# Optimization experiments

Measured on AMD Instinct MI355X. Metric: run time of the kernel, lower is better.

## Reference

```python
import jax, jax.numpy as jnp
import numpy as np

D_MODEL = 256
N_LAYERS = 2
EXPAND = 2
D_INNER = EXPAND * D_MODEL  # 512
D_STATE = 16
D_CONV = 4
DT_RANK = max(1, D_MODEL // 16)  # 16


def _selective_scan(x, dt, B, C, A, D):
    # x, dt: [b, l, d]   B, C: [b, l, n]   A: [d, n]   D: [d]
    dA = jnp.exp(jnp.einsum('bld,dn->bldn', dt, A))          # discretized state matrix
    dBx = jnp.einsum('bld,bln,bld->bldn', dt, B, x)           # dt * B * u

    def step(h, inp):
        dA_t, dBx_t, C_t = inp                                 # [b,d,n],[b,d,n],[b,n]
        h = dA_t * h + dBx_t
        y = jnp.einsum('bdn,bn->bd', h, C_t)
        return h, y

    h0 = jnp.zeros((x.shape[0], A.shape[0], A.shape[1]), x.dtype)
    _, ys = jax.lax.scan(step, h0, (jnp.moveaxis(dA, 1, 0),
                                    jnp.moveaxis(dBx, 1, 0),
                                    jnp.moveaxis(C, 1, 0)))
    return jnp.moveaxis(ys, 0, 1) + x * D                      # [b, l, d]


def _mamba_block(z, in_w, conv_w, conv_b, xp_w, dt_w, dt_b, A_log, Dp, out_w):
    b, l, _ = z.shape
    xz = z @ in_w.T                                            # [b, l, 2*d_inner]
    x, gate = jnp.split(xz, 2, axis=-1)
    # causal depthwise conv1d over time
    xt = jnp.transpose(x, (0, 2, 1))                            # [b, d_inner, l]
    xt = jax.lax.conv_general_dilated(
        xt, conv_w[:, None, :], window_strides=(1,),
        padding=[(D_CONV - 1, 0)], feature_group_count=D_INNER)
    x = jax.nn.silu(jnp.transpose(xt, (0, 2, 1)) + conv_b)      # [b, l, d_inner]
    x_dbl = x @ xp_w.T                                          # [b, l, dt_rank + 2*d_state]
    dt, Bm, Cm = jnp.split(x_dbl, [DT_RANK, DT_RANK + D_STATE], axis=-1)
    dt = jax.nn.softplus(dt @ dt_w.T + dt_b)                    # [b, l, d_inner]
    A = -jnp.exp(A_log)                                         # [d_inner, d_state]
    y = _selective_scan(x, dt, Bm, Cm, A, Dp)
    y = y * jax.nn.silu(gate)
    return y @ out_w.T                                          # [b, l, d_model]


def setup_inputs() -> dict:
    key = jax.random.key(0)
    ks = jax.random.split(key, 9)
    B, L = 2, 4096
    z = jax.random.normal(ks[0], (B, L, D_MODEL), jnp.float32)
    s = 0.02
    in_proj_w = jax.random.normal(ks[1], (N_LAYERS, 2 * D_INNER, D_MODEL), jnp.float32) * s
    conv_w = jax.random.normal(ks[2], (N_LAYERS, D_INNER, D_CONV), jnp.float32) * 0.2
    conv_b = jnp.zeros((N_LAYERS, D_INNER), jnp.float32)
    x_proj_w = jax.random.normal(ks[3], (N_LAYERS, DT_RANK + 2 * D_STATE, D_INNER), jnp.float32) * s
    dt_proj_w = jax.random.normal(ks[4], (N_LAYERS, D_INNER, DT_RANK), jnp.float32) * 0.1
    dt_proj_b = jax.random.uniform(ks[5], (N_LAYERS, D_INNER), jnp.float32, -4.0, -2.0)
    A_log = jnp.log(jnp.broadcast_to(jnp.arange(1, D_STATE + 1, dtype=jnp.float32),
                                     (N_LAYERS, D_INNER, D_STATE)))
    D_param = jnp.ones((N_LAYERS, D_INNER), jnp.float32)
    out_proj_w = jax.random.normal(ks[6], (N_LAYERS, D_MODEL, D_INNER), jnp.float32) * s
    return {"z": z, "in_proj_w": in_proj_w, "conv_w": conv_w, "conv_b": conv_b,
            "x_proj_w": x_proj_w, "dt_proj_w": dt_proj_w, "dt_proj_b": dt_proj_b,
            "A_log": A_log, "D_param": D_param, "out_proj_w": out_proj_w}


def reference(z, in_proj_w, conv_w, conv_b, x_proj_w, dt_proj_w, dt_proj_b,
              A_log, D_param, out_proj_w):
    for i in range(N_LAYERS):
        z = _mamba_block(z, in_proj_w[i], conv_w[i], conv_b[i], x_proj_w[i],
                         dt_proj_w[i], dt_proj_b[i], A_log[i], D_param[i], out_proj_w[i])
    return z
```

## Files before the change

### kernel.cpp

```cpp
#include <hip/hip_runtime.h>
#include <hip/hip_bf16.h>
#include <cstdint>
#include <cstddef>

#define DM   256
#define DI   512
#define DS   16
#define LSEQ 4096
#define BATCH 2
#define BLROWS (BATCH * LSEQ)
#define NCH  128
#define CLEN 32
#define XCP  520

#define OFF_INW 0
#define OFF_XC  0
#define OFF_Z   65536
#define OFF_XD  65536
#define OFF_XX  90880
#define SMEM_SZ 127280

typedef __bf16 bf16x8 __attribute__((ext_vector_type(8)));
typedef float  f32x4  __attribute__((ext_vector_type(4)));
typedef unsigned short u16;
typedef u16 u16x8 __attribute__((ext_vector_type(8)));
typedef u16 u16x4 __attribute__((ext_vector_type(4)));

__device__ __forceinline__ u16 f2bfu(float f) {
    union { float f; unsigned u; } c; c.f = f;
    unsigned u = c.u;
    return (u16)((u + 0x7fffu + ((u >> 16) & 1u)) >> 16);
}
__device__ __forceinline__ float bfu2f(u16 u) {
    union { unsigned u; float f; } c; c.u = ((unsigned)u) << 16; return c.f;
}
__device__ __forceinline__ float siluf(float v) {
    return v * (1.0f / (1.0f + __expf(-v)));
}
__device__ __forceinline__ void gload_lds16(const void* g, void* l) {
    __builtin_amdgcn_global_load_lds(
        (const __attribute__((address_space(1))) unsigned int*)g,
        (__attribute__((address_space(3))) unsigned int*)l, 16, 0, 0);
}

#define N_INW  (2*1024*256)
#define N_OUTW (2*256*512)
#define N_XPW  (2*64*512)
#define N_Z    (BLROWS*DM)
__global__ __launch_bounds__(256) void cast_all_k(
    const float* __restrict__ in_w, const float* __restrict__ out_w,
    const float* __restrict__ xp_w, const float* __restrict__ z,
    u16* __restrict__ inw_bf, u16* __restrict__ outw_bf,
    u16* __restrict__ xpw_bf, u16* __restrict__ z_bf) {
    int i = blockIdx.x * 256 + threadIdx.x;
    if (i < N_INW) {
        inw_bf[i] = f2bfu(in_w[i]);
    } else if (i < N_INW + N_OUTW) {
        int j = i - N_INW;
        outw_bf[j] = f2bfu(out_w[j]);
    } else if (i < N_INW + N_OUTW + N_XPW) {
        int j = i - (N_INW + N_OUTW);
        int k = j & 511, o = (j >> 9) & 63, l = j >> 15;
        xpw_bf[j] = f2bfu((o < 48) ? xp_w[(l * 48 + o) * 512 + k] : 0.0f);
    } else {
        int j = i - (N_INW + N_OUTW + N_XPW);
        z_bf[j] = f2bfu(z[j]);
    }
}

__global__ __launch_bounds__(512) void fused_a_k(
    const u16* __restrict__ zin, const u16* __restrict__ inw,
    const float* __restrict__ cw, const float* __restrict__ cb,
    const __bf16* __restrict__ xpw,
    const float* __restrict__ dtw, const float* __restrict__ dtb,
    const float* __restrict__ Alog,
    u16* __restrict__ xcb, u16* __restrict__ dtob, u16* __restrict__ gateb,
    float* __restrict__ BCg, u16* __restrict__ Pb, u16* __restrict__ Sb) {
    __shared__ __align__(16) char smem[SMEM_SZ];
    u16*  inw_s = (u16*)(smem + OFF_INW);
    u16*  z_s   = (u16*)(smem + OFF_Z);
    u16*  xx_s  = (u16*)(smem + OFF_XX);
    u16*  xc_s  = (u16*)(smem + OFF_XC);
    float* xd_s = (float*)(smem + OFF_XD);
    int tid = threadIdx.x;
    int c = blockIdx.x, b = blockIdx.y;
    int bl0 = b * LSEQ + c * CLEN;
    int wave = tid >> 6, lane = tid & 63;
    int row = lane & 15, q = lane >> 4;
    int d = tid;

    for (int idx = tid; idx < 48 * 32; idx += 512) {
        int r = idx >> 5, c8 = idx & 31;
        u16x8 v = {0,0,0,0,0,0,0,0};
        if (r < 35 && (c > 0 || r >= 3))
            v = *(const u16x8*)(zin + (size_t)(bl0 - 3 + r) * DM + c8 * 8);
        *(u16x8*)(z_s + r * 264 + c8 * 8) = v;
    }
    __syncthreads();

    for (int g = 0; g < 8; ++g) {
        {
            int pos = lane & 31, roff = lane >> 5;
            #pragma unroll
            for (int i = 0; i < 8; ++i) {
                int r_abs = wave * 16 + i * 2 + roff;
                int chunk = (pos - r_abs) & 31;
                gload_lds16(inw + (size_t)(g * 128 + r_abs) * 256 + chunk * 8,
                            inw_s + (wave * 16 + i * 2) * 256);
            }
        }
        __syncthreads();
        f32x4 acc[3] = {};
        #pragma unroll
        for (int kb = 0; kb < 8; ++kb) {
            int cidx = kb * 4 + q;
            int r_abs = wave * 16 + row;
            int pos = (cidx + r_abs) & 31;
            bf16x8 bb = *(const bf16x8*)(inw_s + r_abs * 256 + pos * 8);
            #pragma unroll
            for (int mt = 0; mt < 3; ++mt) {
                bf16x8 a = *(const bf16x8*)(z_s + (mt*16 + row) * 264 + kb*32 + q*8);
                acc[mt] = __builtin_amdgcn_mfma_f32_16x16x32_bf16(a, bb, acc[mt], 0, 0, 0);
            }
        }
        __syncthreads();
        int col = g * 128 + wave * 16 + row;
        #pragma unroll
        for (int mt = 0; mt < 3; ++mt)
            #pragma unroll
            for (int r = 0; r < 4; ++r) {
                int grow = mt * 16 + q * 4 + r;
                if (g < 4) {
                    if (grow < 35) xx_s[grow * XCP + col] = f2bfu(acc[mt][r]);
                } else {
                    int t = grow - 3;
                    if (t >= 0 && t < CLEN)
                        gateb[(size_t)(bl0 + t) * DI + (col - 512)] = f2bfu(acc[mt][r]);
                }
            }
    }
    __syncthreads();

    {
        float w0 = cw[d*4], w1 = cw[d*4+1], w2 = cw[d*4+2], w3 = cw[d*4+3];
        float bias = cb[d];
        float xm3 = bfu2f(xx_s[0*XCP + d]);
        float xm2 = bfu2f(xx_s[1*XCP + d]);
        float xm1 = bfu2f(xx_s[2*XCP + d]);
        #pragma unroll 4
        for (int t = 0; t < CLEN; ++t) {
            float xcur = bfu2f(xx_s[(t + 3) * XCP + d]);
            float v = siluf(fmaf(w0, xm3, fmaf(w1, xm2, fmaf(w2, xm1, fmaf(w3, xcur, bias)))));
            u16 vb = f2bfu(v);
            xc_s[t * XCP + d] = vb;
            xcb[(size_t)(bl0 + t) * DI + d] = vb;
            xm3 = xm2; xm2 = xm1; xm1 = xcur;
        }
    }
    __syncthreads();

    {
        int mt = wave & 1, nt = wave >> 1;
        f32x4 acc = {0.f, 0.f, 0.f, 0.f};
        #pragma unroll
        for (int kb = 0; kb < 16; ++kb) {
            bf16x8 a = *(const bf16x8*)&xc_s[(mt*16 + row) * XCP + kb*32 + q*8];
            bf16x8 bb = *(const bf16x8*)(xpw + (size_t)(nt*16 + row) * 512 + kb*32 + q*8);
            acc = __builtin_amdgcn_mfma_f32_16x16x32_bf16(a, bb, acc, 0, 0, 0);
        }
        #pragma unroll
        for (int r = 0; r < 4; ++r)
            xd_s[(mt*16 + q*4 + r) * 68 + nt*16 + row] = acc[r];
    }
    __syncthreads();

    for (int i = tid; i < CLEN * 32; i += 512) {
        int t = i >> 5, cc = i & 31;
        BCg[((size_t)(b*NCH + c) * CLEN + t) * 32 + cc] = xd_s[t*68 + 16 + cc];
    }

    {
        float dtwr[16];
        const f32x4* w4 = (const f32x4*)(dtw + (size_t)d * 16);
        #pragma unroll
        for (int g = 0; g < 4; ++g) { f32x4 v = w4[g];
            dtwr[g*4] = v[0]; dtwr[g*4+1] = v[1]; dtwr[g*4+2] = v[2]; dtwr[g*4+3] = v[3]; }
        float dtbv = dtb[d];
        float Ac[16];
        const f32x4* a4 = (const f32x4*)(Alog + (size_t)d * 16);
        #pragma unroll
        for (int g = 0; g < 4; ++g) { f32x4 v = a4[g];
            #pragma unroll
            for (int j = 0; j < 4; ++j) Ac[g*4+j] = -__expf(v[j]); }
        bool fastp = true;
        #pragma unroll
        for (int n = 1; n < 16; ++n)
            fastp = fastp && (fabsf(Ac[n] - (float)(n+1) * Ac[0]) <= 1e-4f * fabsf(Ac[n]));
        float p[16], s[16];
        #pragma unroll
        for (int n = 0; n < 16; ++n) { p[n] = 1.0f; s[n] = 0.0f; }
        for (int t = 0; t < CLEN; ++t) {
            float acc = dtbv;
            #pragma unroll
            for (int r = 0; r < 16; ++r) acc = fmaf(xd_s[t*68 + r], dtwr[r], acc);
            float dtv = (acc > 20.0f) ? acc : logf(1.0f + __expf(acc));
            dtob[(size_t)(bl0 + t) * DI + d] = f2bfu(dtv);
            float xv = bfu2f(xc_s[t * XCP + d]);
            float dx = dtv * xv;
            float an[16];
            if (fastp) {
                float a0 = __expf(dtv * Ac[0]);
                an[0] = a0;
                #pragma unroll
                for (int n = 1; n < 16; ++n) an[n] = an[n-1] * a0;
            } else {
                #pragma unroll
                for (int n = 0; n < 16; ++n) an[n] = __expf(dtv * Ac[n]);
            }
            #pragma unroll
            for (int n = 0; n < 16; ++n) {
                s[n] = fmaf(an[n], s[n], xd_s[t*68 + 16 + n] * dx);
                p[n] *= an[n];
            }
        }
        size_t base = ((size_t)(b*NCH + c) * DI + d) * 16;
        u16x8 pv0, pv1, sv0, sv1;
        #pragma unroll
        for (int n = 0; n < 8; ++n) {
            pv0[n] = f2bfu(p[n]);   pv1[n] = f2bfu(p[8+n]);
            sv0[n] = f2bfu(s[n]);   sv1[n] = f2bfu(s[8+n]);
        }
        *(u16x8*)(Pb + base)     = pv0;  *(u16x8*)(Pb + base + 8) = pv1;
        *(u16x8*)(Sb + base)     = sv0;  *(u16x8*)(Sb + base + 8) = sv1;
    }
}

__global__ __launch_bounds__(256) void scanB_k(
    const u16* __restrict__ Pb, const u16* __restrict__ Sb,
    float* __restrict__ H) {
    int i = blockIdx.x * 256 + threadIdx.x;
    int b = i >> 11, j4 = i & 2047;
    f32x4 h = {0.f, 0.f, 0.f, 0.f};
    for (int c = 0; c < NCH; ++c) {
        size_t i4 = (size_t)(b*NCH + c) * 2048 + j4;
        u16x4 pv = ((const u16x4*)Pb)[i4];
        u16x4 sv = ((const u16x4*)Sb)[i4];
        ((f32x4*)H)[i4] = h;
        #pragma unroll
        for (int j = 0; j < 4; ++j) h[j] = fmaf(bfu2f(pv[j]), h[j], bfu2f(sv[j]));
    }
}

__global__ __launch_bounds__(512) void fused_c_k(
    const u16* __restrict__ xcb, const u16* __restrict__ dtob,
    const float* __restrict__ BCg, const float* __restrict__ H,
    const float* __restrict__ Alog, const float* __restrict__ Dp,
    const u16* __restrict__ gateb, const __bf16* __restrict__ outw,
    u16* __restrict__ Ob, float* __restrict__ Of) {
    __shared__ u16 y_s[CLEN * XCP];
    __shared__ float BCs[CLEN * 32];
    int tid = threadIdx.x;
    int c = blockIdx.x, b = blockIdx.y;
    int bl0 = b * LSEQ + c * CLEN;
    int d = tid;

    for (int i = tid; i < CLEN * 32; i += 512)
        BCs[i] = BCg[(size_t)(b*NCH + c) * (CLEN*32) + i];

    float Ac[16], h[16];
    {
        const f32x4* a4 = (const f32x4*)(Alog + (size_t)d * 16);
        const f32x4* h4 = (const f32x4*)(H + ((size_t)(b*NCH + c) * DI + d) * 16);
        #pragma unroll
        for (int g = 0; g < 4; ++g) {
            f32x4 av = a4[g]; f32x4 hv = h4[g];
            #pragma unroll
            for (int j = 0; j < 4; ++j) { Ac[g*4+j] = -__expf(av[j]); h[g*4+j] = hv[j]; }
        }
    }
    bool fastp = true;
    #pragma unroll
    for (int n = 1; n < 16; ++n)
        fastp = fastp && (fabsf(Ac[n] - (float)(n+1) * Ac[0]) <= 1e-4f * fabsf(Ac[n]));
    float Dv = Dp[d];
    __syncthreads();

    #pragma unroll 4
    for (int t = 0; t < CLEN; ++t) {
        float dtv = bfu2f(dtob[(size_t)(bl0 + t) * DI + d]);
        float xv  = bfu2f(xcb[(size_t)(bl0 + t) * DI + d]);
        float gv  = bfu2f(gateb[(size_t)(bl0 + t) * DI + d]);
        float dx = dtv * xv;
        float an[16];
        if (fastp) {
            float a0 = __expf(dtv * Ac[0]);
            an[0] = a0;
            #pragma unroll
            for (int n = 1; n < 16; ++n) an[n] = an[n-1] * a0;
        } else {
            #pragma unroll
            for (int n = 0; n < 16; ++n) an[n] = __expf(dtv * Ac[n]);
        }
        float y = 0.f;
        #pragma unroll
        for (int n = 0; n < 16; ++n) {
            h[n] = fmaf(an[n], h[n], BCs[t*32 + n] * dx);
            y = fmaf(h[n], BCs[t*32 + 16 + n], y);
        }
        float yv = fmaf(xv, Dv, y) * siluf(gv);
        y_s[t * XCP + d] = f2bfu(yv);
    }
    __syncthreads();

    {
        int wave = tid >> 6, lane = tid & 63;
        int row = lane & 15, q = lane >> 4;
        int mt = wave & 1, ng = wave >> 1;
        f32x4 acc[4] = {};
        #pragma unroll
        for (int kb = 0; kb < 16; ++kb) {
            bf16x8 a = *(const bf16x8*)&y_s[(mt*16 + row) * XCP + kb*32 + q*8];
            #pragma unroll
            for (int ni = 0; ni < 4; ++ni) {
                bf16x8 bb = *(const bf16x8*)(outw +
                    (size_t)(ng*64 + ni*16 + row) * 512 + kb*32 + q*8);
                acc[ni] = __builtin_amdgcn_mfma_f32_16x16x32_bf16(a, bb, acc[ni], 0, 0, 0);
            }
        }
        #pragma unroll
        for (int r = 0; r < 4; ++r) {
            size_t gr = (size_t)(bl0 + mt*16 + q*4 + r) * DM;
            #pragma unroll
            for (int ni = 0; ni < 4; ++ni) {
                int gc = ng*64 + ni*16 + row;
                if (Ob) Ob[gr + gc] = f2bfu(acc[ni][r]);
                else    Of[gr + gc] = acc[ni][r];
            }
        }
    }
}

extern "C" void kernel_launch(void* const* d_in, const int* in_sizes, int n_in,
                              void* d_out, int out_size, void* d_ws, size_t ws_size,
                              hipStream_t stream) {
    (void)in_sizes; (void)n_in; (void)out_size; (void)ws_size;
    const float* z_in   = (const float*)d_in[0];
    const float* in_w   = (const float*)d_in[1];
    const float* conv_w = (const float*)d_in[2];
    const float* conv_b = (const float*)d_in[3];
    const float* xp_w   = (const float*)d_in[4];
    const float* dt_w   = (const float*)d_in[5];
    const float* dt_b   = (const float*)d_in[6];
    const float* A_log  = (const float*)d_in[7];
    const float* D_par  = (const float*)d_in[8];
    const float* out_w  = (const float*)d_in[9];
    float* outp = (float*)d_out;

    char* p = (char*)d_ws;
    auto alloc = [&](size_t bytes) { char* r = p; p += (bytes + 255) & ~(size_t)255; return r; };
    u16* z_bf    = (u16*)alloc((size_t)BLROWS*DM*2);
    u16* z2_bf   = (u16*)alloc((size_t)BLROWS*DM*2);
    u16* xc_bf   = (u16*)alloc((size_t)BLROWS*DI*2);
    u16* dt_bf   = (u16*)alloc((size_t)BLROWS*DI*2);
    u16* gate_bf = (u16*)alloc((size_t)BLROWS*DI*2);
    u16* inw_bf  = (u16*)alloc((size_t)2*1024*256*2);
    u16* outw_bf = (u16*)alloc((size_t)2*256*512*2);
    u16* xpw_bf  = (u16*)alloc((size_t)2*64*512*2);
    float* BCg   = (float*)alloc((size_t)BATCH*NCH*CLEN*32*4);
    u16* Pbuf    = (u16*)alloc((size_t)BATCH*NCH*DI*DS*2);
    u16* Sbuf    = (u16*)alloc((size_t)BATCH*NCH*DI*DS*2);
    float* Hbuf  = (float*)alloc((size_t)BATCH*NCH*DI*DS*4);

    cast_all_k<<<(N_INW + N_OUTW + N_XPW + N_Z)/256, 256, 0, stream>>>(
        in_w, out_w, xp_w, z_in, inw_bf, outw_bf, xpw_bf, z_bf);

    const u16* zcur = z_bf;
    for (int l = 0; l < 2; ++l) {
        fused_a_k<<<dim3(NCH, BATCH), 512, 0, stream>>>(
            zcur, inw_bf + (size_t)l*1024*256,
            conv_w + (size_t)l*DI*4, conv_b + (size_t)l*DI,
            (const __bf16*)(xpw_bf + (size_t)l*64*512),
            dt_w + (size_t)l*DI*16, dt_b + (size_t)l*DI,
            A_log + (size_t)l*DI*DS,
            xc_bf, dt_bf, gate_bf, BCg, Pbuf, Sbuf);
        scanB_k<<<16, 256, 0, stream>>>(Pbuf, Sbuf, Hbuf);
        fused_c_k<<<dim3(NCH, BATCH), 512, 0, stream>>>(
            xc_bf, dt_bf, BCg, Hbuf,
            A_log + (size_t)l*DI*DS, D_par + (size_t)l*DI,
            gate_bf, (const __bf16*)(outw_bf + (size_t)l*256*512),
            (l == 0) ? z2_bf : nullptr, (l == 1) ? outp : nullptr);
        zcur = z2_bf;
    }
}
```

Baseline: 265.2 us.

## Split in_proj GEMM across two blocks and read weights directly from global

Adds a third grid dimension so the x half and the gate half of the in_proj GEMM run in separate blocks, with the gate blocks returning early. Weight tiles are now read straight from global memory into registers instead of being staged through LDS with global_load_lds, which removes the per-group barriers. LDS size drops from about 127KB to 72KB and the padding strides change to avoid bank conflicts, which should allow more resident blocks and more parallelism. The cost is redundant loading of the z tile by both halves and uncoalesced, uncached weight reads from global memory.

Result: no change. 261.4 us (-1.4%).

```diff
diff --git a/kernel.cpp b/kernel.cpp
--- a/kernel.cpp
+++ b/kernel.cpp
@@ -11,14 +11,14 @@
 #define BLROWS (BATCH * LSEQ)
 #define NCH  128
 #define CLEN 32
-#define XCP  520
-
-#define OFF_INW 0
-#define OFF_XC  0
-#define OFF_Z   65536
-#define OFF_XD  65536
-#define OFF_XX  90880
-#define SMEM_SZ 127280
+#define XCP  536
+#define ZSP  272
+
+#define OFF_XX  0
+#define OFF_XD  0
+#define OFF_Z   37520
+#define OFF_XC  37520
+#define SMEM_SZ 71824
 
 typedef __bf16 bf16x8 __attribute__((ext_vector_type(8)));
 typedef float  f32x4  __attribute__((ext_vector_type(4)));
@@ -36,11 +36,6 @@
 }
 __device__ __forceinline__ float siluf(float v) {
     return v * (1.0f / (1.0f + __expf(-v)));
-}
-__device__ __forceinline__ void gload_lds16(const void* g, void* l) {
-    __builtin_amdgcn_global_load_lds(
-        (const __attribute__((address_space(1))) unsigned int*)g,
-        (__attribute__((address_space(3))) unsigned int*)l, 16, 0, 0);
 }
 
 #define N_INW  (2*1024*256)
@@ -77,13 +72,12 @@
     u16* __restrict__ xcb, u16* __restrict__ dtob, u16* __restrict__ gateb,
     float* __restrict__ BCg, u16* __restrict__ Pb, u16* __restrict__ Sb) {
     __shared__ __align__(16) char smem[SMEM_SZ];
-    u16*  inw_s = (u16*)(smem + OFF_INW);
     u16*  z_s   = (u16*)(smem + OFF_Z);
     u16*  xx_s  = (u16*)(smem + OFF_XX);
     u16*  xc_s  = (u16*)(smem + OFF_XC);
     float* xd_s = (float*)(smem + OFF_XD);
     int tid = threadIdx.x;
-    int c = blockIdx.x, b = blockIdx.y;
+    int c = blockIdx.x, b = blockIdx.y, half = blockIdx.z;
     int bl0 = b * LSEQ + c * CLEN;
     int wave = tid >> 6, lane = tid & 63;
     int row = lane & 15, q = lane >> 4;
@@ -94,51 +88,38 @@
         u16x8 v = {0,0,0,0,0,0,0,0};
         if (r < 35 && (c > 0 || r >= 3))
             v = *(const u16x8*)(zin + (size_t)(bl0 - 3 + r) * DM + c8 * 8);
-        *(u16x8*)(z_s + r * 264 + c8 * 8) = v;
-    }
-    __syncthreads();
-
-    for (int g = 0; g < 8; ++g) {
-        {
-            int pos = lane & 31, roff = lane >> 5;
-            #pragma unroll
-            for (int i = 0; i < 8; ++i) {
-                int r_abs = wave * 16 + i * 2 + roff;
-                int chunk = (pos - r_abs) & 31;
-                gload_lds16(inw + (size_t)(g * 128 + r_abs) * 256 + chunk * 8,
-                            inw_s + (wave * 16 + i * 2) * 256);
-            }
-        }
-        __syncthreads();
+        *(u16x8*)(z_s + r * ZSP + c8 * 8) = v;
+    }
+    __syncthreads();
+
+    for (int g = 0; g < 4; ++g) {
         f32x4 acc[3] = {};
+        const u16* wp = inw + (size_t)(half*512 + g*128 + wave*16 + row) * 256;
         #pragma unroll
         for (int kb = 0; kb < 8; ++kb) {
-            int cidx = kb * 4 + q;
-            int r_abs = wave * 16 + row;
-            int pos = (cidx + r_abs) & 31;
-            bf16x8 bb = *(const bf16x8*)(inw_s + r_abs * 256 + pos * 8);
+            bf16x8 bb = *(const bf16x8*)(wp + kb*32 + q*8);
             #pragma unroll
             for (int mt = 0; mt < 3; ++mt) {
-                bf16x8 a = *(const bf16x8*)(z_s + (mt*16 + row) * 264 + kb*32 + q*8);
+                bf16x8 a = *(const bf16x8*)(z_s + (mt*16 + row) * ZSP + kb*32 + q*8);
                 acc[mt] = __builtin_amdgcn_mfma_f32_16x16x32_bf16(a, bb, acc[mt], 0, 0, 0);
             }
         }
-        __syncthreads();
         int col = g * 128 + wave * 16 + row;
         #pragma unroll
         for (int mt = 0; mt < 3; ++mt)
             #pragma unroll
             for (int r = 0; r < 4; ++r) {
                 int grow = mt * 16 + q * 4 + r;
-                if (g < 4) {
+                if (half == 0) {
                     if (grow < 35) xx_s[grow * XCP + col] = f2bfu(acc[mt][r]);
                 } else {
                     int t = grow - 3;
                     if (t >= 0 && t < CLEN)
-                        gateb[(size_t)(bl0 + t) * DI + (col - 512)] = f2bfu(acc[mt][r]);
+                        gateb[(size_t)(bl0 + t) * DI + col] = f2bfu(acc[mt][r]);
                 }
             }
     }
+    if (half == 1) return;
     __syncthreads();
 
     {
@@ -376,7 +357,7 @@
 
     const u16* zcur = z_bf;
     for (int l = 0; l < 2; ++l) {
-        fused_a_k<<<dim3(NCH, BATCH), 512, 0, stream>>>(
+        fused_a_k<<<dim3(NCH, BATCH, 2), 512, 0, stream>>>(
             zcur, inw_bf + (size_t)l*1024*256,
             conv_w + (size_t)l*DI*4, conv_b + (size_t)l*DI,
             (const __bf16*)(xpw_bf + (size_t)l*64*512),
```
